# Kernel tuning notes

Measured on AMD Instinct MI355X. Metric: run time of the kernel, lower is better.

Reference implementation:

```python
import jax, jax.numpy as jnp
import numpy as np

VOCAB = 21128; EMBED = 768; D_MODEL = 256; H = 100; NTAGS = 21; B = 32; T = 256


def setup_inputs() -> dict:
    key = jax.random.key(0)
    ks = jax.random.split(key, 18)
    n = lambda k, s, sc=0.05: jax.random.normal(k, s, dtype=jnp.float32) * sc
    return {
        "words": jax.random.randint(ks[0], (B, T), 0, VOCAB),
        "target": jax.random.randint(ks[1], (B, T), 0, NTAGS),
        "embed_table": n(ks[2], (VOCAB, EMBED), 1.0),
        "in_fc_w": n(ks[3], (D_MODEL, EMBED)),
        "in_fc_b": n(ks[4], (D_MODEL,)),
        "Wih0": n(ks[5], (2, 4 * H, D_MODEL)),
        "Whh0": n(ks[6], (2, 4 * H, H)),
        "bih0": n(ks[7], (2, 4 * H)),
        "bhh0": n(ks[8], (2, 4 * H)),
        "Wih1": n(ks[9], (2, 4 * H, 2 * H)),
        "Whh1": n(ks[10], (2, 4 * H, H)),
        "bih1": n(ks[11], (2, 4 * H)),
        "bhh1": n(ks[12], (2, 4 * H)),
        "out_w": n(ks[13], (NTAGS, 2 * H)),
        "out_b": n(ks[14], (NTAGS,)),
        "trans": n(ks[15], (NTAGS, NTAGS)),
        "start_s": n(ks[16], (NTAGS,)),
        "end_s": n(ks[17], (NTAGS,)),
    }


def _lstm_dir(x, Wih, Whh, bih, bhh, reverse):
    # x: (T, B, D); torch LSTM gate order i, f, g, o
    Bsz, Hd = x.shape[1], Whh.shape[1]
    pre = jnp.einsum('tbd,gd->tbg', x, Wih) + bih  # precompute input projection

    def step(carry, p):
        h, c = carry
        g = p + h @ Whh.T + bhh
        i, f, gg, o = jnp.split(g, 4, axis=-1)
        c = jax.nn.sigmoid(f) * c + jax.nn.sigmoid(i) * jnp.tanh(gg)
        h = jax.nn.sigmoid(o) * jnp.tanh(c)
        return (h, c), h

    init = (jnp.zeros((Bsz, Hd), x.dtype), jnp.zeros((Bsz, Hd), x.dtype))
    _, hs = jax.lax.scan(step, init, pre, reverse=reverse)
    return hs


def _bilstm(x, layers):
    h = x
    for (Wih, Whh, bih, bhh) in layers:  # fixed small loop over num_layers
        f = _lstm_dir(h, Wih[0], Whh[0], bih[0], bhh[0], False)
        b = _lstm_dir(h, Wih[1], Whh[1], bih[1], bhh[1], True)
        h = jnp.concatenate([f, b], axis=-1)
    return h


def _crf_loss(logits, tags, mask, trans, start_s, end_s):
    # fastNLP ConditionalRandomField loss: normalizer - gold_score, per batch elem
    lt = jnp.swapaxes(logits, 0, 1)          # (T, B, N)
    tt = tags.T                               # (T, B)
    mt = mask.T.astype(logits.dtype)          # (T, B)
    alpha0 = lt[0] + start_s

    def step(alpha, inp):
        emit, m = inp
        tmp = alpha[:, :, None] + trans[None] + emit[:, None, :]  # (B, N, N)
        new = jax.nn.logsumexp(tmp, axis=1)
        return jnp.where(m[:, None] > 0, new, alpha), None

    alpha, _ = jax.lax.scan(step, alpha0, (lt[1:], mt[1:]))
    normalizer = jax.nn.logsumexp(alpha + end_s, axis=1)  # (B,)

    emit_sc = jnp.take_along_axis(lt, tt[..., None], axis=2)[..., 0] * mt
    trans_sc = trans[tt[:-1], tt[1:]] * mt[1:]
    seq_lens = mask.sum(axis=1)
    last_idx = jnp.maximum(seq_lens - 1, 0)
    last_tags = tags[jnp.arange(tags.shape[0]), last_idx]
    gold = emit_sc.sum(0) + trans_sc.sum(0) + start_s[tt[0]] + end_s[last_tags]
    return normalizer - gold


def reference(words, target, embed_table, in_fc_w, in_fc_b, Wih0, Whh0, bih0, bhh0,
              Wih1, Whh1, bih1, bhh1, out_w, out_b, trans, start_s, end_s):
    mask = words != 0
    x = embed_table[words]                       # (B, T, E)
    x = x @ in_fc_w.T + in_fc_b                  # (B, T, D)
    x = jnp.swapaxes(x, 0, 1)                    # (T, B, D)
    h = _bilstm(x, [(Wih0, Whh0, bih0, bhh0), (Wih1, Whh1, bih1, bhh1)])
    h = jnp.swapaxes(h, 0, 1)                    # (B, T, 2H); dropout is identity at eval
    logits = jax.nn.log_softmax(h @ out_w.T + out_b, axis=-1)
    return _crf_loss(logits, target, mask, trans, start_s, end_s)  # (B,)
```

## Files before the change

kernel.cpp:

```cpp
#include <hip/hip_runtime.h>
#include <hip/hip_bf16.h>

#define VOCAB 21128
#define EMBED 768
#define DMODEL 256
#define HID 100
#define NTAGS 21
#define BB 32
#define TT 256
#define NTOK (BB*TT)

typedef float f32x4 __attribute__((ext_vector_type(4)));
typedef unsigned int u32x4 __attribute__((ext_vector_type(4)));

__device__ __forceinline__ float sigm(float x) { return 1.0f / (1.0f + __expf(-x)); }
__device__ __forceinline__ float tanh_(float x) { return 2.0f / (1.0f + __expf(-2.0f * x)) - 1.0f; }

__device__ __forceinline__ unsigned int bfr(float x) {
    unsigned int u = __float_as_uint(x);
    return (u + 0x7fffu + ((u >> 16) & 1u)) >> 16;
}
__device__ __forceinline__ unsigned int bfpack(float lo, float hi) {
    return (bfr(hi) << 16) | bfr(lo);
}

__global__ __launch_bounds__(256) void gemm_bias(
    const float* __restrict__ A, int lda,
    const float* __restrict__ B, int ldb,
    const float* __restrict__ bias1, const float* __restrict__ bias2,
    float* __restrict__ C, int ldc,
    int M, int N, int K,
    const int* __restrict__ gatherWords, int permGates)
{
    __shared__ float As[8][64];
    __shared__ float Bs[8][64];
    const int row0 = blockIdx.x * 64;
    const int col0 = blockIdx.y * 64;
    const int tid = threadIdx.x;
    const int tx = tid & 15;
    const int ty = tid >> 4;
    float acc[4][4] = {};

    for (int k0 = 0; k0 < K; k0 += 8) {
        if (tid < 128) {
            int r = tid >> 1, q = tid & 1;
            int grow = row0 + r;
            const float* ap;
            if (gatherWords) {
                int widx = gatherWords[(grow & 31) * TT + (grow >> 5)];
                ap = A + (size_t)widx * lda;
            } else {
                ap = A + (size_t)grow * lda;
            }
            float4 v = *(const float4*)(ap + k0 + q * 4);
            As[q*4+0][r] = v.x; As[q*4+1][r] = v.y;
            As[q*4+2][r] = v.z; As[q*4+3][r] = v.w;
        } else {
            int f = tid - 128;
            int r = f >> 1, q = f & 1;
            int gcol = col0 + r;
            float4 v = make_float4(0.f, 0.f, 0.f, 0.f);
            if (gcol < N) {
                int src = gcol;
                if (permGates) {
                    int d2 = (gcol >= 400) ? 1 : 0;
                    int rr = gcol - d2 * 400;
                    src = d2 * 400 + (rr & 3) * 100 + (rr >> 2);
                }
                v = *(const float4*)(B + (size_t)src * ldb + k0 + q * 4);
            }
            Bs[q*4+0][r] = v.x; Bs[q*4+1][r] = v.y;
            Bs[q*4+2][r] = v.z; Bs[q*4+3][r] = v.w;
        }
        __syncthreads();
        #pragma unroll
        for (int kk = 0; kk < 8; ++kk) {
            float4 av = *(const float4*)&As[kk][ty * 4];
            float4 bv = *(const float4*)&Bs[kk][tx * 4];
            acc[0][0] += av.x * bv.x; acc[0][1] += av.x * bv.y;
            acc[0][2] += av.x * bv.z; acc[0][3] += av.x * bv.w;
            acc[1][0] += av.y * bv.x; acc[1][1] += av.y * bv.y;
            acc[1][2] += av.y * bv.z; acc[1][3] += av.y * bv.w;
            acc[2][0] += av.z * bv.x; acc[2][1] += av.z * bv.y;
            acc[2][2] += av.z * bv.z; acc[2][3] += av.z * bv.w;
            acc[3][0] += av.w * bv.x; acc[3][1] += av.w * bv.y;
            acc[3][2] += av.w * bv.z; acc[3][3] += av.w * bv.w;
        }
        __syncthreads();
    }

    float bb_[4];
    #pragma unroll
    for (int jj = 0; jj < 4; ++jj) {
        int gcol = col0 + tx * 4 + jj;
        float bv = 0.f;
        if (gcol < N) {
            int src = gcol;
            if (permGates) {
                int d2 = (gcol >= 400) ? 1 : 0;
                int rr = gcol - d2 * 400;
                src = d2 * 400 + (rr & 3) * 100 + (rr >> 2);
            }
            bv = bias1[src];
            if (bias2) bv += bias2[src];
        }
        bb_[jj] = bv;
    }
    #pragma unroll
    for (int ii = 0; ii < 4; ++ii) {
        int grow = row0 + ty * 4 + ii;
        #pragma unroll
        for (int jj = 0; jj < 4; ++jj) {
            int gcol = col0 + tx * 4 + jj;
            if (gcol < N) C[(size_t)grow * ldc + gcol] = acc[ii][jj] + bb_[jj];
        }
    }
}

#define STASH_FRAG(DD, F, A0,A1,A2,A3) { \
    int tile = 4*wave + DD; if (tile > 24) tile = 24; \
    int row16 = 16*tile + m16; \
    const float* srcp = Whh + (size_t)(dir*400 + (row16 & 3)*100 + (row16 >> 2)) * HID; \
    const int k0 = 32*F + 8*g4; \
    f32x4 fa = {0.f,0.f,0.f,0.f}, fb = {0.f,0.f,0.f,0.f}; \
    if (k0 < HID) fa = *(const f32x4*)(srcp + k0); \
    if (k0 + 4 < HID) fb = *(const f32x4*)(srcp + k0 + 4); \
    unsigned p0 = bfpack(fa.x, fa.y), p1 = bfpack(fa.z, fa.w); \
    unsigned p2 = bfpack(fb.x, fb.y), p3 = bfpack(fb.z, fb.w); \
    asm volatile("v_accvgpr_write_b32 a" #A0 ", %0\n\t" \
                 "v_accvgpr_write_b32 a" #A1 ", %1\n\t" \
                 "v_accvgpr_write_b32 a" #A2 ", %2\n\t" \
                 "v_accvgpr_write_b32 a" #A3 ", %3" \
                 :: "v"(p0), "v"(p1), "v"(p2), "v"(p3) \
                 : "a" #A0, "a" #A1, "a" #A2, "a" #A3); }

#define MF(ACC, BF, A0, A3) \
    asm volatile("v_mfma_f32_16x16x32_bf16 %0, a[" #A0 ":" #A3 "], %1, %0" \
                 : "+v"(ACC) : "v"(BF));

__global__ __launch_bounds__(448, 1) void lstm_mfma(
    const float* __restrict__ pre,
    const float* __restrict__ Whh,
    float* __restrict__ hout)
{
    const int dir = blockIdx.x >> 5;
    const int b = blockIdx.x & 31;
    const int tid = threadIdx.x;
    const int wave = tid >> 6;
    const int lane = tid & 63;
    const int m16 = lane & 15;
    const int g4 = lane >> 4;
    const int d = lane & 3;

    __shared__ alignas(16) unsigned short h16[2][128];

    STASH_FRAG(0,0, 0,1,2,3)    STASH_FRAG(0,1, 4,5,6,7)
    STASH_FRAG(0,2, 8,9,10,11)  STASH_FRAG(0,3, 12,13,14,15)
    STASH_FRAG(1,0, 16,17,18,19) STASH_FRAG(1,1, 20,21,22,23)
    STASH_FRAG(1,2, 24,25,26,27) STASH_FRAG(1,3, 28,29,30,31)
    STASH_FRAG(2,0, 32,33,34,35) STASH_FRAG(2,1, 36,37,38,39)
    STASH_FRAG(2,2, 40,41,42,43) STASH_FRAG(2,3, 44,45,46,47)
    STASH_FRAG(3,0, 48,49,50,51) STASH_FRAG(3,1, 52,53,54,55)
    STASH_FRAG(3,2, 56,57,58,59) STASH_FRAG(3,3, 60,61,62,63)

    if (tid < 128) { h16[0][tid] = 0; h16[1][tid] = 0; }

    int tl0 = 4*wave + 0; if (tl0 > 24) tl0 = 24;
    int tl1 = 4*wave + 1; if (tl1 > 24) tl1 = 24;
    int tl2 = 4*wave + 2; if (tl2 > 24) tl2 = 24;
    int tl3 = 4*wave + 3; if (tl3 > 24) tl3 = 24;
    const int po0 = dir*400 + 16*tl0 + 4*g4;
    const int po1 = dir*400 + 16*tl1 + 4*g4;
    const int po2 = dir*400 + 16*tl2 + 4*g4;
    const int po3 = dir*400 + 16*tl3 + 4*g4;
    int my_tile = 4*wave + d; if (my_tile > 24) my_tile = 24;
    const int my_u = my_tile*4 + g4;
    const bool writer = ((lane & 12) == 0) && (wave < 6 || d == 0);

    float c = 0.f;
    __syncthreads();

    const int i0 = (dir ? (TT-1) : 0) * BB + b;
    f32x4 pc0 = *(const f32x4*)(pre + (size_t)i0*800 + po0);
    f32x4 pc1 = *(const f32x4*)(pre + (size_t)i0*800 + po1);
    f32x4 pc2 = *(const f32x4*)(pre + (size_t)i0*800 + po2);
    f32x4 pc3 = *(const f32x4*)(pre + (size_t)i0*800 + po3);

    for (int s = 0; s < TT; ++s) {
        const int t = dir ? (TT-1-s) : s;
        const int i = t * BB + b;

        f32x4 pn0, pn1, pn2, pn3;
        if (s + 1 < TT) {
            const int tn = dir ? (TT-2-s) : (s+1);
            const size_t ib = (size_t)(tn * BB + b) * 800;
            pn0 = *(const f32x4*)(pre + ib + po0);
            pn1 = *(const f32x4*)(pre + ib + po1);
            pn2 = *(const f32x4*)(pre + ib + po2);
            pn3 = *(const f32x4*)(pre + ib + po3);
        } else { pn0 = pc0; pn1 = pc1; pn2 = pc2; pn3 = pc3; }

        const u32x4* hb = (const u32x4*)&h16[s & 1][0];
        u32x4 bf0 = hb[g4];
        u32x4 bf1 = hb[4 + g4];
        u32x4 bf2 = hb[8 + g4];
        u32x4 bf3 = hb[12 + g4];

        f32x4 acc0 = pc0, acc1 = pc1, acc2 = pc2, acc3 = pc3;

        asm volatile("s_nop 1");
        MF(acc0, bf0, 0, 3)   MF(acc1, bf0, 16, 19) MF(acc2, bf0, 32, 35) MF(acc3, bf0, 48, 51)
        MF(acc0, bf1, 4, 7)   MF(acc1, bf1, 20, 23) MF(acc2, bf1, 36, 39) MF(acc3, bf1, 52, 55)
        MF(acc0, bf2, 8, 11)  MF(acc1, bf2, 24, 27) MF(acc2, bf2, 40, 43) MF(acc3, bf2, 56, 59)
        MF(acc0, bf3, 12, 15) MF(acc1, bf3, 28, 31) MF(acc2, bf3, 44, 47) MF(acc3, bf3, 60, 63)
        asm volatile("s_nop 7\n\ts_nop 7");

        f32x4 sel = (d == 0) ? acc0 : (d == 1) ? acc1 : (d == 2) ? acc2 : acc3;
        float igt = sigm(sel.x);
        float fgt = sigm(sel.y);
        float ggt = tanh_(sel.z);
        float ogt = sigm(sel.w);
        c = fgt * c + igt * ggt;
        float h = ogt * tanh_(c);

        if (writer) {
            h16[(s + 1) & 1][my_u] = (unsigned short)bfr(h);
            hout[(size_t)i * 200 + dir * HID + my_u] = h;
        }
        __syncthreads();
        pc0 = pn0; pc1 = pn1; pc2 = pn2; pc3 = pn3;
    }
}

__global__ __launch_bounds__(256) void logits_lsm(
    const float* __restrict__ h1,
    const float* __restrict__ out_w,
    const float* __restrict__ out_b,
    float* __restrict__ logits)
{
    const int lane = threadIdx.x & 63;
    const int wid = (blockIdx.x * 256 + threadIdx.x) >> 6;
    const int half = lane >> 5;
    const int n = lane & 31;
    const int i = wid * 2 + half;
    if (i >= NTOK) return;

    float acc = -1e30f;
    if (n < NTAGS) {
        acc = out_b[n];
        const float4* hr = (const float4*)(h1 + (size_t)i * 200);
        const float4* wr = (const float4*)(out_w + (size_t)n * 200);
        #pragma unroll
        for (int e = 0; e < 50; ++e) {
            float4 h4 = hr[e], w4 = wr[e];
            acc += h4.x * w4.x + h4.y * w4.y + h4.z * w4.z + h4.w * w4.w;
        }
    }
    float m = acc;
    for (int off = 16; off > 0; off >>= 1) m = fmaxf(m, __shfl_xor(m, off, 32));
    float ex = (n < NTAGS) ? __expf(acc - m) : 0.f;
    float s = ex;
    for (int off = 16; off > 0; off >>= 1) s += __shfl_xor(s, off, 32);
    if (n < NTAGS) logits[(size_t)i * NTAGS + n] = acc - m - __logf(s);
}

__global__ __launch_bounds__(64) void crf_kernel(
    const float* __restrict__ logits,
    const int* __restrict__ words,
    const int* __restrict__ target,
    const float* __restrict__ trans,
    const float* __restrict__ start_s,
    const float* __restrict__ end_s,
    float* __restrict__ out)
{
    const int b = blockIdx.x;
    const int j = threadIdx.x;

    float tcol[NTAGS];
    #pragma unroll
    for (int i = 0; i < NTAGS; ++i) tcol[i] = (j < NTAGS) ? trans[i * NTAGS + j] : 0.f;

    float alpha = (j < NTAGS) ? (logits[(size_t)(0 * BB + b) * NTAGS + j] + start_s[j]) : -1e30f;

    for (int t = 1; t < TT; ++t) {
        bool mt = (words[b * TT + t] != 0);
        if (mt) {
            float v[NTAGS];
            float mx = -1e30f;
            #pragma unroll
            for (int i2 = 0; i2 < NTAGS; ++i2) {
                float ai = __shfl(alpha, i2, 64);
                v[i2] = ai + tcol[i2];
                mx = fmaxf(mx, v[i2]);
            }
            float s = 0.f;
            #pragma unroll
            for (int i2 = 0; i2 < NTAGS; ++i2) s += __expf(v[i2] - mx);
            float na = mx + __logf(s) + logits[(size_t)(t * BB + b) * NTAGS + j];
            alpha = (j < NTAGS) ? na : -1e30f;
        }
    }

    float val = (j < NTAGS) ? (alpha + end_s[j]) : -1e30f;
    float mx = val;
    for (int off = 32; off > 0; off >>= 1) mx = fmaxf(mx, __shfl_xor(mx, off, 64));
    float s = (j < NTAGS) ? __expf(val - mx) : 0.f;
    for (int off = 32; off > 0; off >>= 1) s += __shfl_xor(s, off, 64);
    float norm = mx + __logf(s);

    float gold = 0.f, slen = 0.f;
    for (int t = j; t < TT; t += 64) {
        int tg = target[b * TT + t];
        bool m = (words[b * TT + t] != 0);
        if (m) {
            gold += logits[(size_t)(t * BB + b) * NTAGS + tg];
            slen += 1.f;
            if (t >= 1) gold += trans[target[b * TT + t - 1] * NTAGS + tg];
        }
    }
    for (int off = 32; off > 0; off >>= 1) {
        gold += __shfl_xor(gold, off, 64);
        slen += __shfl_xor(slen, off, 64);
    }
    if (j == 0) {
        int len = (int)slen;
        int last = (len > 0) ? (len - 1) : 0;
        int last_tag = target[b * TT + last];
        gold += start_s[target[b * TT + 0]] + end_s[last_tag];
        out[b] = norm - gold;
    }
}

extern "C" void kernel_launch(void* const* d_in, const int* in_sizes, int n_in,
                              void* d_out, int out_size, void* d_ws, size_t ws_size,
                              hipStream_t stream) {
    const int*   words   = (const int*)  d_in[0];
    const int*   target  = (const int*)  d_in[1];
    const float* embed   = (const float*)d_in[2];
    const float* in_fc_w = (const float*)d_in[3];
    const float* in_fc_b = (const float*)d_in[4];
    const float* Wih0    = (const float*)d_in[5];
    const float* Whh0    = (const float*)d_in[6];
    const float* bih0    = (const float*)d_in[7];
    const float* bhh0    = (const float*)d_in[8];
    const float* Wih1    = (const float*)d_in[9];
    const float* Whh1    = (const float*)d_in[10];
    const float* bih1    = (const float*)d_in[11];
    const float* bhh1    = (const float*)d_in[12];
    const float* out_w   = (const float*)d_in[13];
    const float* out_b   = (const float*)d_in[14];
    const float* trans   = (const float*)d_in[15];
    const float* start_s = (const float*)d_in[16];
    const float* end_s   = (const float*)d_in[17];
    float* out = (float*)d_out;

    float* ws = (float*)d_ws;
    float* x      = ws;
    float* pre    = ws + 2097152;
    float* h0     = ws + 8650752;
    float* h1     = ws;
    float* logits = ws + 1638400;

    gemm_bias<<<dim3(NTOK / 64, DMODEL / 64), 256, 0, stream>>>(
        embed, EMBED, in_fc_w, EMBED, in_fc_b, nullptr,
        x, DMODEL, NTOK, DMODEL, EMBED, words, 0);

    gemm_bias<<<dim3(NTOK / 64, 13), 256, 0, stream>>>(
        x, DMODEL, Wih0, DMODEL, bih0, bhh0,
        pre, 800, NTOK, 800, DMODEL, nullptr, 1);

    lstm_mfma<<<64, 448, 0, stream>>>(pre, Whh0, h0);

    gemm_bias<<<dim3(NTOK / 64, 13), 256, 0, stream>>>(
        h0, 200, Wih1, 200, bih1, bhh1,
        pre, 800, NTOK, 800, 200, nullptr, 1);

    lstm_mfma<<<64, 448, 0, stream>>>(pre, Whh1, h1);

    logits_lsm<<<NTOK / 8, 256, 0, stream>>>(h1, out_w, out_b, logits);

    crf_kernel<<<BB, 64, 0, stream>>>(logits, words, target, trans, start_s, end_s, out);
}
```

Measured before the change: 686.9 us.

## Move projection GEMMs to bf16 MFMA with double-buffered LDS and deepen LSTM prefetch

```diff
diff --git a/kernel.cpp b/kernel.cpp
--- a/kernel.cpp
+++ b/kernel.cpp
@@ -12,6 +12,7 @@
 
 typedef float f32x4 __attribute__((ext_vector_type(4)));
 typedef unsigned int u32x4 __attribute__((ext_vector_type(4)));
+typedef short s16x8 __attribute__((ext_vector_type(8)));
 
 __device__ __forceinline__ float sigm(float x) { return 1.0f / (1.0f + __expf(-x)); }
 __device__ __forceinline__ float tanh_(float x) { return 2.0f / (1.0f + __expf(-2.0f * x)) - 1.0f; }
@@ -23,77 +24,136 @@
 __device__ __forceinline__ unsigned int bfpack(float lo, float hi) {
     return (bfr(hi) << 16) | bfr(lo);
 }
-
-__global__ __launch_bounds__(256) void gemm_bias(
+__device__ __forceinline__ s16x8 asfrag(u32x4 v) {
+    union { u32x4 u; s16x8 s; } x; x.u = v; return x.s;
+}
+
+__global__ __launch_bounds__(256) void gemm_mfma(
     const float* __restrict__ A, int lda,
     const float* __restrict__ B, int ldb,
     const float* __restrict__ bias1, const float* __restrict__ bias2,
     float* __restrict__ C, int ldc,
-    int M, int N, int K,
+    int N, int K,
     const int* __restrict__ gatherWords, int permGates)
 {
-    __shared__ float As[8][64];
-    __shared__ float Bs[8][64];
-    const int row0 = blockIdx.x * 64;
+    __shared__ unsigned int As_[2][2048];
+    __shared__ unsigned int Bs_[2][1024];
+
+    const int tid = threadIdx.x;
+    const int row0 = blockIdx.x * 128;
     const int col0 = blockIdx.y * 64;
-    const int tid = threadIdx.x;
-    const int tx = tid & 15;
-    const int ty = tid >> 4;
-    float acc[4][4] = {};
-
-    for (int k0 = 0; k0 < K; k0 += 8) {
-        if (tid < 128) {
-            int r = tid >> 1, q = tid & 1;
-            int grow = row0 + r;
-            const float* ap;
-            if (gatherWords) {
-                int widx = gatherWords[(grow & 31) * TT + (grow >> 5)];
-                ap = A + (size_t)widx * lda;
-            } else {
-                ap = A + (size_t)grow * lda;
-            }
-            float4 v = *(const float4*)(ap + k0 + q * 4);
-            As[q*4+0][r] = v.x; As[q*4+1][r] = v.y;
-            As[q*4+2][r] = v.z; As[q*4+3][r] = v.w;
+    const int lane = tid & 63;
+    const int wave = tid >> 6;
+    const int wr = wave >> 1, wc = wave & 1;
+    const int nsteps = (K + 31) >> 5;
+
+    const float* arow[4]; int aoff[4]; int kqA[4];
+    #pragma unroll
+    for (int j = 0; j < 4; ++j) {
+        int v = tid + 256 * j;
+        int row = v >> 3, kq = v & 7;
+        int grow = row0 + row;
+        const float* ap;
+        if (gatherWords) {
+            int widx = gatherWords[(grow & 31) * TT + (grow >> 5)];
+            ap = A + (size_t)widx * lda;
         } else {
-            int f = tid - 128;
-            int r = f >> 1, q = f & 1;
-            int gcol = col0 + r;
-            float4 v = make_float4(0.f, 0.f, 0.f, 0.f);
-            if (gcol < N) {
-                int src = gcol;
-                if (permGates) {
-                    int d2 = (gcol >= 400) ? 1 : 0;
-                    int rr = gcol - d2 * 400;
-                    src = d2 * 400 + (rr & 3) * 100 + (rr >> 2);
-                }
-                v = *(const float4*)(B + (size_t)src * ldb + k0 + q * 4);
-            }
-            Bs[q*4+0][r] = v.x; Bs[q*4+1][r] = v.y;
-            Bs[q*4+2][r] = v.z; Bs[q*4+3][r] = v.w;
+            ap = A + (size_t)grow * lda;
+        }
+        arow[j] = ap + 4 * kq;
+        aoff[j] = (row >> 4) * 256 + (kq >> 1) * 64 + (row & 15) * 4 + (kq & 1) * 2;
+        kqA[j] = kq;
+    }
+    const float* brow[2]; int boff[2]; int bok[2]; int kqB[2];
+    #pragma unroll
+    for (int j = 0; j < 2; ++j) {
+        int v = tid + 256 * j;
+        int r = v >> 3, kq = v & 7;
+        int gcol = col0 + r;
+        bok[j] = (gcol < N);
+        int src = bok[j] ? gcol : 0;
+        if (permGates && bok[j]) {
+            int d2 = (gcol >= 400) ? 1 : 0;
+            int rr = gcol - d2 * 400;
+            src = d2 * 400 + (rr & 3) * 100 + (rr >> 2);
+        }
+        brow[j] = B + (size_t)src * ldb + 4 * kq;
+        boff[j] = (r >> 4) * 256 + (kq >> 1) * 64 + (r & 15) * 4 + (kq & 1) * 2;
+        kqB[j] = kq;
+    }
+
+    {
+        #pragma unroll
+        for (int j = 0; j < 4; ++j) {
+            f32x4 v = {0.f,0.f,0.f,0.f};
+            if (4 * kqA[j] < K) v = *(const f32x4*)(arow[j]);
+            As_[0][aoff[j]]     = bfpack(v.x, v.y);
+            As_[0][aoff[j] + 1] = bfpack(v.z, v.w);
+        }
+        #pragma unroll
+        for (int j = 0; j < 2; ++j) {
+            f32x4 v = {0.f,0.f,0.f,0.f};
+            if (bok[j] && 4 * kqB[j] < K) v = *(const f32x4*)(brow[j]);
+            Bs_[0][boff[j]]     = bfpack(v.x, v.y);
+            Bs_[0][boff[j] + 1] = bfpack(v.z, v.w);
+        }
+    }
+    __syncthreads();
+
+    f32x4 acc[4][2] = {};
+
+    for (int s = 0; s < nsteps; ++s) {
+        const int cur = s & 1, nxt = cur ^ 1;
+
+        f32x4 la[4], lb[2];
+        if (s + 1 < nsteps) {
+            const int kb = (s + 1) * 32;
+            #pragma unroll
+            for (int j = 0; j < 4; ++j) {
+                la[j] = (f32x4){0.f,0.f,0.f,0.f};
+                if (kb + 4 * kqA[j] < K) la[j] = *(const f32x4*)(arow[j] + kb);
+            }
+            #pragma unroll
+            for (int j = 0; j < 2; ++j) {
+                lb[j] = (f32x4){0.f,0.f,0.f,0.f};
+                if (bok[j] && kb + 4 * kqB[j] < K) lb[j] = *(const f32x4*)(brow[j] + kb);
+            }
+        }
+
+        u32x4 af[4], bf[2];
+        #pragma unroll
+        for (int mt = 0; mt < 4; ++mt)
+            af[mt] = *(const u32x4*)&As_[cur][(4 * wr + mt) * 256 + lane * 4];
+        #pragma unroll
+        for (int nt = 0; nt < 2; ++nt)
+            bf[nt] = *(const u32x4*)&Bs_[cur][(2 * wc + nt) * 256 + lane * 4];
+        #pragma unroll
+        for (int mt = 0; mt < 4; ++mt)
+            #pragma unroll
+            for (int nt = 0; nt < 2; ++nt)
+                acc[mt][nt] = __builtin_amdgcn_mfma_f32_16x16x32_bf16(
+                    asfrag(af[mt]), asfrag(bf[nt]), acc[mt][nt], 0, 0, 0);
+
+        if (s + 1 < nsteps) {
+            #pragma unroll
+            for (int j = 0; j < 4; ++j) {
+                As_[nxt][aoff[j]]     = bfpack(la[j].x, la[j].y);
+                As_[nxt][aoff[j] + 1] = bfpack(la[j].z, la[j].w);
+            }
+            #pragma unroll
+            for (int j = 0; j < 2; ++j) {
+                Bs_[nxt][boff[j]]     = bfpack(lb[j].x, lb[j].y);
+                Bs_[nxt][boff[j] + 1] = bfpack(lb[j].z, lb[j].w);
+            }
         }
         __syncthreads();
-        #pragma unroll
-        for (int kk = 0; kk < 8; ++kk) {
-            float4 av = *(const float4*)&As[kk][ty * 4];
-            float4 bv = *(const float4*)&Bs[kk][tx * 4];
-            acc[0][0] += av.x * bv.x; acc[0][1] += av.x * bv.y;
-            acc[0][2] += av.x * bv.z; acc[0][3] += av.x * bv.w;
-            acc[1][0] += av.y * bv.x; acc[1][1] += av.y * bv.y;
-            acc[1][2] += av.y * bv.z; acc[1][3] += av.y * bv.w;
-            acc[2][0] += av.z * bv.x; acc[2][1] += av.z * bv.y;
-            acc[2][2] += av.z * bv.z; acc[2][3] += av.z * bv.w;
-            acc[3][0] += av.w * bv.x; acc[3][1] += av.w * bv.y;
-            acc[3][2] += av.w * bv.z; acc[3][3] += av.w * bv.w;
-        }
-        __syncthreads();
-    }
-
-    float bb_[4];
+    }
+
+    const int r4 = (lane >> 4) * 4;
+    const int cl = lane & 15;
     #pragma unroll
-    for (int jj = 0; jj < 4; ++jj) {
-        int gcol = col0 + tx * 4 + jj;
-        float bv = 0.f;
+    for (int nt = 0; nt < 2; ++nt) {
+        int gcol = col0 + (2 * wc + nt) * 16 + cl;
         if (gcol < N) {
             int src = gcol;
             if (permGates) {
@@ -101,18 +161,15 @@
                 int rr = gcol - d2 * 400;
                 src = d2 * 400 + (rr & 3) * 100 + (rr >> 2);
             }
-            bv = bias1[src];
+            float bv = bias1[src];
             if (bias2) bv += bias2[src];
-        }
-        bb_[jj] = bv;
-    }
-    #pragma unroll
-    for (int ii = 0; ii < 4; ++ii) {
-        int grow = row0 + ty * 4 + ii;
-        #pragma unroll
-        for (int jj = 0; jj < 4; ++jj) {
-            int gcol = col0 + tx * 4 + jj;
-            if (gcol < N) C[(size_t)grow * ldc + gcol] = acc[ii][jj] + bb_[jj];
+            #pragma unroll
+            for (int mt = 0; mt < 4; ++mt) {
+                int grow = row0 + (4 * wr + mt) * 16 + r4;
+                #pragma unroll
+                for (int r = 0; r < 4; ++r)
+                    C[(size_t)(grow + r) * ldc + gcol] = acc[mt][nt][r] + bv;
+            }
         }
     }
 }
@@ -138,6 +195,39 @@
     asm volatile("v_mfma_f32_16x16x32_bf16 %0, a[" #A0 ":" #A3 "], %1, %0" \
                  : "+v"(ACC) : "v"(BF));
 
+#define LSTM_STEP(P0,P1,P2,P3, S) { \
+    const int t_ = dir ? (TT-1-(S)) : (S); \
+    const int i_ = t_ * BB + b; \
+    const u32x4* hb_ = (const u32x4*)&h16[(S) & 1][0]; \
+    u32x4 bf0 = hb_[g4], bf1 = hb_[4+g4], bf2 = hb_[8+g4], bf3 = hb_[12+g4]; \
+    f32x4 acc0 = P0, acc1 = P1, acc2 = P2, acc3 = P3; \
+    if ((S) + 2 < TT) { \
+        const int tn_ = dir ? (TT-3-(S)) : ((S)+2); \
+        const size_t ib_ = (size_t)(tn_ * BB + b) * 800; \
+        P0 = *(const f32x4*)(pre + ib_ + po0); \
+        P1 = *(const f32x4*)(pre + ib_ + po1); \
+        P2 = *(const f32x4*)(pre + ib_ + po2); \
+        P3 = *(const f32x4*)(pre + ib_ + po3); \
+    } \
+    asm volatile("s_nop 1"); \
+    MF(acc0, bf0, 0, 3)   MF(acc1, bf0, 16, 19) MF(acc2, bf0, 32, 35) MF(acc3, bf0, 48, 51) \
+    MF(acc0, bf1, 4, 7)   MF(acc1, bf1, 20, 23) MF(acc2, bf1, 36, 39) MF(acc3, bf1, 52, 55) \
+    MF(acc0, bf2, 8, 11)  MF(acc1, bf2, 24, 27) MF(acc2, bf2, 40, 43) MF(acc3, bf2, 56, 59) \
+    MF(acc0, bf3, 12, 15) MF(acc1, bf3, 28, 31) MF(acc2, bf3, 44, 47) MF(acc3, bf3, 60, 63) \
+    asm volatile("s_nop 7\n\ts_nop 7"); \
+    f32x4 sel = (d == 0) ? acc0 : (d == 1) ? acc1 : (d == 2) ? acc2 : acc3; \
+    float igt = sigm(sel.x); \
+    float fgt = sigm(sel.y); \
+    float ggt = tanh_(sel.z); \
+    float ogt = sigm(sel.w); \
+    c = fgt * c + igt * ggt; \
+    float h = ogt * tanh_(c); \
+    if (writer) { \
+        h16[((S) + 1) & 1][my_u] = (unsigned short)bfr(h); \
+        hout[(size_t)i_ * 200 + dir * HID + my_u] = h; \
+    } \
+    __syncthreads(); }
+
 __global__ __launch_bounds__(448, 1) void lstm_mfma(
     const float* __restrict__ pre,
     const float* __restrict__ Whh,
@@ -180,55 +270,20 @@
     float c = 0.f;
     __syncthreads();
 
-    const int i0 = (dir ? (TT-1) : 0) * BB + b;
-    f32x4 pc0 = *(const f32x4*)(pre + (size_t)i0*800 + po0);
-    f32x4 pc1 = *(const f32x4*)(pre + (size_t)i0*800 + po1);
-    f32x4 pc2 = *(const f32x4*)(pre + (size_t)i0*800 + po2);
-    f32x4 pc3 = *(const f32x4*)(pre + (size_t)i0*800 + po3);
-
-    for (int s = 0; s < TT; ++s) {
-        const int t = dir ? (TT-1-s) : s;
-        const int i = t * BB + b;
-
-        f32x4 pn0, pn1, pn2, pn3;
-        if (s + 1 < TT) {
-            const int tn = dir ? (TT-2-s) : (s+1);
-            const size_t ib = (size_t)(tn * BB + b) * 800;
-            pn0 = *(const f32x4*)(pre + ib + po0);
-            pn1 = *(const f32x4*)(pre + ib + po1);
-            pn2 = *(const f32x4*)(pre + ib + po2);
-            pn3 = *(const f32x4*)(pre + ib + po3);
-        } else { pn0 = pc0; pn1 = pc1; pn2 = pc2; pn3 = pc3; }
-
-        const u32x4* hb = (const u32x4*)&h16[s & 1][0];
-        u32x4 bf0 = hb[g4];
-        u32x4 bf1 = hb[4 + g4];
-        u32x4 bf2 = hb[8 + g4];
-        u32x4 bf3 = hb[12 + g4];
-
-        f32x4 acc0 = pc0, acc1 = pc1, acc2 = pc2, acc3 = pc3;
-
-        asm volatile("s_nop 1");
-        MF(acc0, bf0, 0, 3)   MF(acc1, bf0, 16, 19) MF(acc2, bf0, 32, 35) MF(acc3, bf0, 48, 51)
-        MF(acc0, bf1, 4, 7)   MF(acc1, bf1, 20, 23) MF(acc2, bf1, 36, 39) MF(acc3, bf1, 52, 55)
-        MF(acc0, bf2, 8, 11)  MF(acc1, bf2, 24, 27) MF(acc2, bf2, 40, 43) MF(acc3, bf2, 56, 59)
-        MF(acc0, bf3, 12, 15) MF(acc1, bf3, 28, 31) MF(acc2, bf3, 44, 47) MF(acc3, bf3, 60, 63)
-        asm volatile("s_nop 7\n\ts_nop 7");
-
-        f32x4 sel = (d == 0) ? acc0 : (d == 1) ? acc1 : (d == 2) ? acc2 : acc3;
-        float igt = sigm(sel.x);
-        float fgt = sigm(sel.y);
-        float ggt = tanh_(sel.z);
-        float ogt = sigm(sel.w);
-        c = fgt * c + igt * ggt;
-        float h = ogt * tanh_(c);
-
-        if (writer) {
-            h16[(s + 1) & 1][my_u] = (unsigned short)bfr(h);
-            hout[(size_t)i * 200 + dir * HID + my_u] = h;
-        }
-        __syncthreads();
-        pc0 = pn0; pc1 = pn1; pc2 = pn2; pc3 = pn3;
+    const size_t ib0 = (size_t)((dir ? (TT-1) : 0) * BB + b) * 800;
+    const size_t ib1 = (size_t)((dir ? (TT-2) : 1) * BB + b) * 800;
+    f32x4 pa0 = *(const f32x4*)(pre + ib0 + po0);
+    f32x4 pa1 = *(const f32x4*)(pre + ib0 + po1);
+    f32x4 pa2 = *(const f32x4*)(pre + ib0 + po2);
+    f32x4 pa3 = *(const f32x4*)(pre + ib0 + po3);
+    f32x4 pb0 = *(const f32x4*)(pre + ib1 + po0);
+    f32x4 pb1 = *(const f32x4*)(pre + ib1 + po1);
+    f32x4 pb2 = *(const f32x4*)(pre + ib1 + po2);
+    f32x4 pb3 = *(const f32x4*)(pre + ib1 + po3);
+
+    for (int s = 0; s < TT; s += 2) {
+        LSTM_STEP(pa0, pa1, pa2, pa3, s)
+        LSTM_STEP(pb0, pb1, pb2, pb3, s + 1)
     }
 }
 
@@ -361,19 +416,19 @@
     float* h1     = ws;
     float* logits = ws + 1638400;
 
-    gemm_bias<<<dim3(NTOK / 64, DMODEL / 64), 256, 0, stream>>>(
+    gemm_mfma<<<dim3(64, 4), 256, 0, stream>>>(
         embed, EMBED, in_fc_w, EMBED, in_fc_b, nullptr,
-        x, DMODEL, NTOK, DMODEL, EMBED, words, 0);
-
-    gemm_bias<<<dim3(NTOK / 64, 13), 256, 0, stream>>>(
+        x, DMODEL, DMODEL, EMBED, words, 0);
+
+    gemm_mfma<<<dim3(64, 13), 256, 0, stream>>>(
         x, DMODEL, Wih0, DMODEL, bih0, bhh0,
-        pre, 800, NTOK, 800, DMODEL, nullptr, 1);
+        pre, 800, 800, DMODEL, nullptr, 1);
 
     lstm_mfma<<<64, 448, 0, stream>>>(pre, Whh0, h0);
 
-    gemm_bias<<<dim3(NTOK / 64, 13), 256, 0, stream>>>(
+    gemm_mfma<<<dim3(64, 13), 256, 0, stream>>>(
         h0, 200, Wih1, 200, bih1, bhh1,
-        pre, 800, NTOK, 800, 200, nullptr, 1);
+        pre, 800, 800, 200, nullptr, 1);
 
     lstm_mfma<<<64, 448, 0, stream>>>(pre, Whh1, h1);
 
```

New measurement: 619.0 us. 1.11x faster.
